# Performance work log

Measured on AMD Instinct MI355X. Metric: run time of the kernel, lower is better.

The kernel has to match this reference:

```python
import jax, jax.numpy as jnp
import numpy as np

B, S, D = 32, 512, 512
H, DK, DV, DFF = 8, 64, 64, 2048
TEMP = float(np.sqrt(DK))  # d_k ** 0.5
COS_EPS = 1e-8             # torch.cosine_similarity eps
LN_EPS = 1e-5


def _layernorm(x, g, b):
    mu = jnp.mean(x, axis=-1, keepdims=True)
    var = jnp.var(x, axis=-1, keepdims=True)
    return (x - mu) * jax.lax.rsqrt(var + LN_EPS) * g + b


def setup_inputs() -> dict:
    key = jax.random.key(0)
    ks = jax.random.split(key, 12)
    s = 0.02
    return {
        "x": jax.random.normal(ks[0], (B, S, D), dtype=jnp.float32),
        "w_q": jax.random.normal(ks[1], (D, H * DK), dtype=jnp.float32) * s,
        "w_k": jax.random.normal(ks[2], (D, H * DK), dtype=jnp.float32) * s,
        "w_v": jax.random.normal(ks[3], (D, H * DV), dtype=jnp.float32) * s,
        "w_o": jax.random.normal(ks[4], (H * DV, D), dtype=jnp.float32) * s,
        "w_ff1": jax.random.normal(ks[5], (D, DFF), dtype=jnp.float32) * s,
        "b_ff1": jnp.zeros((DFF,), dtype=jnp.float32),
        "w_ff2": jax.random.normal(ks[6], (DFF, D), dtype=jnp.float32) * s,
        "b_ff2": jnp.zeros((D,), dtype=jnp.float32),
        "g1": jnp.ones((D,), dtype=jnp.float32),
        "b1": jnp.zeros((D,), dtype=jnp.float32),
        "g2": jnp.ones((D,), dtype=jnp.float32),
        "b2": jnp.zeros((D,), dtype=jnp.float32),
    }


def reference(x, w_q, w_k, w_v, w_o, w_ff1, b_ff1, w_ff2, b_ff2, g1, b1, g2, b2):
    b, s, _ = x.shape
    # projections -> [b, h, s, d]
    q = (x @ w_q).reshape(b, s, H, DK).transpose(0, 2, 1, 3)
    k = (x @ w_k).reshape(b, s, H, DK).transpose(0, 2, 1, 3)
    v = (x @ w_v).reshape(b, s, H, DV).transpose(0, 2, 1, 3)
    # cosine-similarity attention: dot(q,k) / max(||q||*||k||, eps) / temperature
    scores = jnp.einsum("bhqd,bhkd->bhqk", q, k)
    nq = jnp.linalg.norm(q, axis=-1)  # [b,h,s]
    nk = jnp.linalg.norm(k, axis=-1)
    denom = jnp.maximum(nq[:, :, :, None] * nk[:, :, None, :], COS_EPS)
    attn = jax.nn.softmax(scores / denom / TEMP, axis=-1)
    out = jnp.einsum("bhqk,bhkd->bhqd", attn, v)  # [b,h,s,dv]
    out = out.transpose(0, 2, 1, 3).reshape(b, s, H * DV) @ w_o
    # residual + LN1
    h1 = _layernorm(x + out, g1, b1)
    # FFN
    ffn = jax.nn.relu(h1 @ w_ff1 + b_ff1) @ w_ff2 + b_ff2
    # residual + LN2
    return _layernorm(h1 + ffn, g2, b2)
```

## Files before the change

### kernel.cpp

```cpp
#include <hip/hip_runtime.h>
#include <cmath>

typedef __bf16 bf16x8 __attribute__((ext_vector_type(8)));
typedef float  floatx4 __attribute__((ext_vector_type(4)));

#define LN_EPS 1e-5f
#define COS_EPS 1e-8f
#define INV_TEMP 0.125f

static const int Mrows = 16384;

__device__ __forceinline__ void gload_lds16(const void* g, void* l) {
  __builtin_amdgcn_global_load_lds(
      (const __attribute__((address_space(1))) void*)g,
      (__attribute__((address_space(3))) void*)l, 16, 0, 0);
}

__global__ __launch_bounds__(256) void convert_bf16(const float* __restrict__ src,
                                                    __bf16* __restrict__ dst, int n4) {
  int i = blockIdx.x * 256 + threadIdx.x;
  if (i < n4) {
    float4 v = ((const float4*)src)[i];
    dst[i * 4 + 0] = (__bf16)v.x;
    dst[i * 4 + 1] = (__bf16)v.y;
    dst[i * 4 + 2] = (__bf16)v.z;
    dst[i * 4 + 3] = (__bf16)v.w;
  }
}

__global__ __launch_bounds__(256) void tr_kernel(const float* __restrict__ src,
                                                 __bf16* __restrict__ dst,
                                                 int R, int C) {
  __shared__ __bf16 til[64][72];
  const int tid = threadIdx.x;
  const int bx = blockIdx.x;
  const int by = blockIdx.y;
  const float* s = src + (size_t)(by * 64) * C + bx * 64;
  int r = tid >> 4, c4 = (tid & 15) * 4;
  for (int p = 0; p < 4; ++p) {
    int rr = r + p * 16;
    float4 v = *(const float4*)(s + (size_t)rr * C + c4);
    til[c4 + 0][rr] = (__bf16)v.x;
    til[c4 + 1][rr] = (__bf16)v.y;
    til[c4 + 2][rr] = (__bf16)v.z;
    til[c4 + 3][rr] = (__bf16)v.w;
  }
  __syncthreads();
  __bf16* d = dst + (size_t)(bx * 64) * R + by * 64;
  int orow = tid >> 3, oc8 = (tid & 7) * 8;
  for (int p = 0; p < 2; ++p) {
    int rr = orow + p * 32;
    *(bf16x8*)(d + (size_t)rr * R + oc8) = *(const bf16x8*)(&til[rr][oc8]);
  }
}

template <int EPI>
__global__ __launch_bounds__(256) void gemm_bt(const __bf16* __restrict__ A,
                                               const __bf16* __restrict__ Bt,
                                               void* __restrict__ Cv,
                                               void* __restrict__ Cv2,
                                               const float* __restrict__ bias,
                                               float* __restrict__ norms,
                                               int nbn, int Ndim, int Kdim, int kspan) {
  __shared__ __align__(16) __bf16 As[128 * 64];
  __shared__ __align__(16) __bf16 Bs[128 * 64];
  const int tid = threadIdx.x;
  const int wave = tid >> 6, lane = tid & 63;
  const int l15 = lane & 15, quad = lane >> 4;
  const int id = blockIdx.x;
  const int xcd = id & 7, t = id >> 3;
  const int nblk = t % nbn, mblk = (t / nbn) * 8 + xcd;
  const int m0 = mblk * 128, n0 = nblk * 128;
  const int k0 = blockIdx.z * kspan;
  const int wrow = (wave >> 1) * 64, wcol = (wave & 1) * 64;
  const int rs = lane >> 3;
  const int swz_st = ((lane & 7) ^ rs) * 8;
  const int s7 = l15 & 7;

  floatx4 zero = {0.f, 0.f, 0.f, 0.f};
  floatx4 acc[4][4];
  for (int i = 0; i < 4; ++i)
    for (int j = 0; j < 4; ++j) acc[i][j] = zero;

  for (int kt = k0; kt < k0 + kspan; kt += 64) {
    __syncthreads();
    for (int c = 0; c < 8; ++c) {
      int g = wave * 8 + c;
      const __bf16* src;
      __bf16* dst;
      if (g < 16) {
        int row = m0 + g * 8 + rs;
        src = A + (size_t)row * Kdim + kt + swz_st;
        dst = As + g * 512;
      } else {
        int g2 = g - 16;
        int row = n0 + g2 * 8 + rs;
        src = Bt + (size_t)row * Kdim + kt + swz_st;
        dst = Bs + g2 * 512;
      }
      gload_lds16(src, dst + lane * 8);
    }
    __syncthreads();
    for (int hh = 0; hh < 2; ++hh) {
      int ko = ((hh * 4 + quad) ^ s7) * 8;
      bf16x8 a[4], b[4];
      for (int i = 0; i < 4; ++i)
        a[i] = *(const bf16x8*)(As + (wrow + i * 16 + l15) * 64 + ko);
      for (int j = 0; j < 4; ++j)
        b[j] = *(const bf16x8*)(Bs + (wcol + j * 16 + l15) * 64 + ko);
      for (int i = 0; i < 4; ++i)
        for (int j = 0; j < 4; ++j)
          acc[i][j] = __builtin_amdgcn_mfma_f32_16x16x32_bf16(a[i], b[j], acc[i][j], 0, 0, 0);
    }
  }

  if (EPI == 4) {
    int head_global = (n0 + wcol) >> 6;
    int kind = head_global >> 3;
    if (kind < 2) {
      int h = head_global & 7;
      for (int i = 0; i < 4; ++i)
        for (int r = 0; r < 4; ++r) {
          float sq = 0.f;
          for (int j = 0; j < 4; ++j) {
            float v = acc[i][j][r];
            sq += v * v;
          }
          for (int m = 1; m < 16; m <<= 1) sq += __shfl_xor(sq, m, 64);
          if (l15 == 0) {
            int arow = m0 + wrow + i * 16 + quad * 4 + r;
            int bb = arow >> 9, ss = arow & 511;
            norms[kind * 131072 + ((bb << 3) + h) * 512 + ss] = sqrtf(sq);
          }
        }
    }
  }

  float* outp = (float*)Cv;
  if (EPI == 1 && blockIdx.z != 0) outp = (float*)Cv2;

  for (int i = 0; i < 4; ++i)
    for (int j = 0; j < 4; ++j) {
      int row = m0 + wrow + i * 16 + quad * 4;
      int col = n0 + wcol + j * 16 + l15;
      float bv = (EPI == 2) ? bias[col] : 0.f;
      for (int r = 0; r < 4; ++r) {
        float v = acc[i][j][r];
        size_t idx = (size_t)(row + r) * Ndim + col;
        if (EPI == 4) {
          ((__bf16*)Cv)[idx] = (__bf16)v;
        } else if (EPI == 1) {
          outp[idx] = v;
        } else {
          v += bv;
          v = v > 0.f ? v : 0.f;
          ((__bf16*)Cv)[idx] = (__bf16)v;
        }
      }
    }
}

__global__ __launch_bounds__(256) void vtrans_kernel(const __bf16* __restrict__ qkv,
                                                     __bf16* __restrict__ vtg) {
  __shared__ __align__(16) unsigned short til[64][68];
  const int tid = threadIdx.x;
  const int st = blockIdx.x;
  const int bh = blockIdx.y;
  const int b = bh >> 3, h = bh & 7;
  const unsigned short* src = (const unsigned short*)qkv +
      (size_t)(b * 512 + st * 64) * 1536 + 1024 + h * 64;
  for (int it = 0; it < 2; ++it) {
    int row = it * 32 + (tid >> 3);
    int c8 = (tid & 7) * 8;
    bf16x8 v = *(const bf16x8*)((const __bf16*)src + (size_t)row * 1536 + c8);
    for (int i = 0; i < 8; ++i) til[row][c8 + i] = ((unsigned short*)&v)[i];
  }
  __syncthreads();
  unsigned short* dst = (unsigned short*)vtg + (size_t)bh * 32768 + st * 64;
  for (int it = 0; it < 2; ++it) {
    int d = it * 32 + (tid >> 3);
    int s8 = (tid & 7) * 8;
    unsigned short v[8];
    for (int i = 0; i < 8; ++i) v[i] = til[s8 + i][d];
    *(bf16x8*)(dst + (size_t)d * 512 + s8) = *(bf16x8*)v;
  }
}

__global__ __launch_bounds__(256) void attn_kernel(const __bf16* __restrict__ qkv,
                                                   const __bf16* __restrict__ vtg,
                                                   const float* __restrict__ norms,
                                                   __bf16* __restrict__ out) {
  __shared__ __align__(16) __bf16 Ks[64 * 64];
  __shared__ __align__(16) __bf16 Vs[64 * 64];
  __shared__ __align__(16) __bf16 P[4][16 * 72];
  const int tid = threadIdx.x, wave = tid >> 6, lane = tid & 63;
  const int l15 = lane & 15, quad = lane >> 4;
  const int qh = blockIdx.x;
  const int bh = blockIdx.y;
  const int b = bh >> 3, h = bh & 7;
  const int qbase = qh * 256 + wave * 64;
  const int rs = lane >> 3;
  const int swz_st = ((lane & 7) ^ rs) * 8;
  const int s7 = l15 & 7;

  const __bf16* Qb = qkv + (size_t)(b * 512) * 1536 + h * 64;
  const __bf16* Kb = Qb + 512;
  const __bf16* Vtb = vtg + (size_t)bh * 32768;
  const float* nkbase = norms + 131072 + bh * 512;
  __bf16* Pw = P[wave];

  bf16x8 aq[4][2];
  float nq[4][4];
  for (int ch = 0; ch < 4; ++ch) {
    int qrow = qbase + ch * 16;
    aq[ch][0] = *(const bf16x8*)(Qb + (size_t)(qrow + l15) * 1536 + quad * 8);
    aq[ch][1] = *(const bf16x8*)(Qb + (size_t)(qrow + l15) * 1536 + 32 + quad * 8);
    for (int r = 0; r < 4; ++r) nq[ch][r] = norms[bh * 512 + qrow + quad * 4 + r];
  }

  floatx4 zero = {0.f, 0.f, 0.f, 0.f};
  floatx4 o[4][4];
  float lsum[4][4];
  for (int ch = 0; ch < 4; ++ch)
    for (int jd = 0; jd < 4; ++jd) o[ch][jd] = zero;
  for (int ch = 0; ch < 4; ++ch)
    for (int r = 0; r < 4; ++r) lsum[ch][r] = 0.f;

  for (int kt = 0; kt < 8; ++kt) {
    int s0 = kt * 64;
    __syncthreads();
    for (int c = 0; c < 4; ++c) {
      int g = wave * 4 + c;
      const __bf16* src;
      __bf16* dst;
      if (g < 8) {
        int sk = g * 8 + rs;
        src = Kb + (size_t)(s0 + sk) * 1536 + swz_st;
        dst = Ks + g * 512;
      } else {
        int g2 = g - 8;
        int d = g2 * 8 + rs;
        src = Vtb + (size_t)d * 512 + s0 + swz_st;
        dst = Vs + g2 * 512;
      }
      gload_lds16(src, dst + lane * 8);
    }
    __syncthreads();

    float nk[4];
    for (int j = 0; j < 4; ++j) nk[j] = nkbase[s0 + j * 16 + l15];

    for (int ch = 0; ch < 4; ++ch) {
      floatx4 z[4];
      for (int j = 0; j < 4; ++j) {
        int r64 = (j * 16 + l15) * 64;
        bf16x8 b0 = *(const bf16x8*)(Ks + r64 + ((quad ^ s7) * 8));
        bf16x8 b1 = *(const bf16x8*)(Ks + r64 + (((4 + quad) ^ s7) * 8));
        floatx4 zz = zero;
        zz = __builtin_amdgcn_mfma_f32_16x16x32_bf16(aq[ch][0], b0, zz, 0, 0, 0);
        zz = __builtin_amdgcn_mfma_f32_16x16x32_bf16(aq[ch][1], b1, zz, 0, 0, 0);
        z[j] = zz;
      }
      for (int j = 0; j < 4; ++j)
        for (int r = 0; r < 4; ++r) {
          float den = nq[ch][r] * nk[j];
          den = den > COS_EPS ? den : COS_EPS;
          float p = __expf(z[j][r] * __builtin_amdgcn_rcpf(den) * INV_TEMP);
          lsum[ch][r] += p;
          Pw[(quad * 4 + r) * 72 + j * 16 + l15] = (__bf16)p;
        }
      bf16x8 ap0 = *(const bf16x8*)(Pw + l15 * 72 + quad * 8);
      bf16x8 ap1 = *(const bf16x8*)(Pw + l15 * 72 + 32 + quad * 8);
      for (int jd = 0; jd < 4; ++jd) {
        int r64 = (jd * 16 + l15) * 64;
        bf16x8 v0 = *(const bf16x8*)(Vs + r64 + ((quad ^ s7) * 8));
        bf16x8 v1 = *(const bf16x8*)(Vs + r64 + (((4 + quad) ^ s7) * 8));
        o[ch][jd] = __builtin_amdgcn_mfma_f32_16x16x32_bf16(ap0, v0, o[ch][jd], 0, 0, 0);
        o[ch][jd] = __builtin_amdgcn_mfma_f32_16x16x32_bf16(ap1, v1, o[ch][jd], 0, 0, 0);
      }
    }
  }

  for (int ch = 0; ch < 4; ++ch)
    for (int r = 0; r < 4; ++r) {
      float s = lsum[ch][r];
      for (int m = 1; m < 16; m <<= 1) s += __shfl_xor(s, m, 64);
      lsum[ch][r] = __builtin_amdgcn_rcpf(s);
    }
  for (int ch = 0; ch < 4; ++ch)
    for (int jd = 0; jd < 4; ++jd)
      for (int r = 0; r < 4; ++r) {
        int q = qbase + ch * 16 + quad * 4 + r;
        int d = jd * 16 + l15;
        out[(size_t)(b * 512 + q) * 512 + h * 64 + d] = (__bf16)(o[ch][jd][r] * lsum[ch][r]);
      }
}

template <bool WB>
__global__ __launch_bounds__(256) void resid_ln(const float* __restrict__ X1,
                                                const float* __restrict__ X2,
                                                const float* __restrict__ X3,
                                                const float* __restrict__ bias,
                                                const float* __restrict__ g,
                                                const float* __restrict__ be,
                                                float* __restrict__ outf,
                                                __bf16* __restrict__ outb) {
  int row = blockIdx.x * 4 + (threadIdx.x >> 6);
  int lane = threadIdx.x & 63;
  const float4* r1 = (const float4*)(X1 + (size_t)row * 512);
  const float4* r2 = (const float4*)(X2 + (size_t)row * 512);
  float4 a = r1[lane], b = r2[lane];
  float4 cc = r1[lane + 64], d = r2[lane + 64];
  float v[8] = {a.x + b.x, a.y + b.y, a.z + b.z, a.w + b.w,
                cc.x + d.x, cc.y + d.y, cc.z + d.z, cc.w + d.w};
  if (X3) {
    const float4* r3 = (const float4*)(X3 + (size_t)row * 512);
    float4 e = r3[lane], f = r3[lane + 64];
    v[0] += e.x; v[1] += e.y; v[2] += e.z; v[3] += e.w;
    v[4] += f.x; v[5] += f.y; v[6] += f.z; v[7] += f.w;
  }
  if (bias) {
    float4 q0 = ((const float4*)bias)[lane], q1 = ((const float4*)bias)[lane + 64];
    v[0] += q0.x; v[1] += q0.y; v[2] += q0.z; v[3] += q0.w;
    v[4] += q1.x; v[5] += q1.y; v[6] += q1.z; v[7] += q1.w;
  }
  float s = 0.f, sq = 0.f;
  for (int i = 0; i < 8; ++i) {
    s += v[i];
    sq += v[i] * v[i];
  }
  for (int m = 1; m < 64; m <<= 1) {
    s += __shfl_xor(s, m, 64);
    sq += __shfl_xor(sq, m, 64);
  }
  float mean = s * (1.f / 512.f);
  float var = sq * (1.f / 512.f) - mean * mean;
  float rstd = rsqrtf(var + LN_EPS);
  float4 g0 = ((const float4*)g)[lane], g1 = ((const float4*)g)[lane + 64];
  float4 b0 = ((const float4*)be)[lane], b1 = ((const float4*)be)[lane + 64];
  float gg[8] = {g0.x, g0.y, g0.z, g0.w, g1.x, g1.y, g1.z, g1.w};
  float bb[8] = {b0.x, b0.y, b0.z, b0.w, b1.x, b1.y, b1.z, b1.w};
  float o[8];
  for (int i = 0; i < 8; ++i) o[i] = (v[i] - mean) * rstd * gg[i] + bb[i];
  float4 w0 = {o[0], o[1], o[2], o[3]}, w1 = {o[4], o[5], o[6], o[7]};
  ((float4*)(outf + (size_t)row * 512))[lane] = w0;
  ((float4*)(outf + (size_t)row * 512))[lane + 64] = w1;
  if (WB) {
    __bf16* ob = outb + (size_t)row * 512;
    for (int i = 0; i < 4; ++i) ob[lane * 4 + i] = (__bf16)o[i];
    for (int i = 0; i < 4; ++i) ob[256 + lane * 4 + i] = (__bf16)o[4 + i];
  }
}

extern "C" void kernel_launch(void* const* d_in, const int* in_sizes, int n_in,
                              void* d_out, int out_size, void* d_ws, size_t ws_size,
                              hipStream_t stream) {
  const float* x     = (const float*)d_in[0];
  const float* w_q   = (const float*)d_in[1];
  const float* w_k   = (const float*)d_in[2];
  const float* w_v   = (const float*)d_in[3];
  const float* w_o   = (const float*)d_in[4];
  const float* w_ff1 = (const float*)d_in[5];
  const float* b_ff1 = (const float*)d_in[6];
  const float* w_ff2 = (const float*)d_in[7];
  const float* b_ff2 = (const float*)d_in[8];
  const float* g1    = (const float*)d_in[9];
  const float* b1    = (const float*)d_in[10];
  const float* g2    = (const float*)d_in[11];
  const float* b2    = (const float*)d_in[12];
  float* out = (float*)d_out;

  char* ws = (char*)d_ws;
  size_t off = 0;
  auto alloc = [&](size_t bytes) -> void* {
    void* p = ws + off;
    off += (bytes + 255) & ~(size_t)255;
    return p;
  };
  __bf16* xb     = (__bf16*)alloc((size_t)Mrows * 512 * 2);
  __bf16* wt_qkv = (__bf16*)alloc((size_t)1536 * 512 * 2);
  __bf16* wt_o   = (__bf16*)alloc((size_t)512 * 512 * 2);
  __bf16* wt_ff1 = (__bf16*)alloc((size_t)2048 * 512 * 2);
  __bf16* wt_ff2 = (__bf16*)alloc((size_t)512 * 2048 * 2);
  __bf16* qkv    = (__bf16*)alloc((size_t)Mrows * 1536 * 2);
  float*  norms  = (float*)alloc((size_t)262144 * 4);
  __bf16* attn   = (__bf16*)alloc((size_t)Mrows * 512 * 2);
  float*  proj   = (float*)alloc((size_t)Mrows * 512 * 4);
  float*  h1f    = (float*)alloc((size_t)Mrows * 512 * 4);
  __bf16* h1b    = (__bf16*)alloc((size_t)Mrows * 512 * 2);
  __bf16* mid    = (__bf16*)alloc((size_t)Mrows * 2048 * 2);
  __bf16* vtg    = mid;
  float*  part1  = (float*)qkv;

  convert_bf16<<<8192, 256, 0, stream>>>(x, xb, Mrows * 512 / 4);
  tr_kernel<<<dim3(8, 8), 256, 0, stream>>>(w_q, wt_qkv, 512, 512);
  tr_kernel<<<dim3(8, 8), 256, 0, stream>>>(w_k, wt_qkv + 512 * 512, 512, 512);
  tr_kernel<<<dim3(8, 8), 256, 0, stream>>>(w_v, wt_qkv + 2 * 512 * 512, 512, 512);
  tr_kernel<<<dim3(8, 8), 256, 0, stream>>>(w_o, wt_o, 512, 512);
  tr_kernel<<<dim3(32, 8), 256, 0, stream>>>(w_ff1, wt_ff1, 512, 2048);
  tr_kernel<<<dim3(8, 32), 256, 0, stream>>>(w_ff2, wt_ff2, 2048, 512);

  gemm_bt<4><<<dim3(12 * 128), 256, 0, stream>>>(xb, wt_qkv, qkv, nullptr, nullptr,
                                                 norms, 12, 1536, 512, 512);
  vtrans_kernel<<<dim3(8, 256), 256, 0, stream>>>(qkv, vtg);
  attn_kernel<<<dim3(2, 256), 256, 0, stream>>>(qkv, vtg, norms, attn);
  gemm_bt<1><<<dim3(4 * 128), 256, 0, stream>>>(attn, wt_o, proj, nullptr, nullptr,
                                                nullptr, 4, 512, 512, 512);
  resid_ln<true><<<4096, 256, 0, stream>>>(x, proj, nullptr, nullptr, g1, b1, h1f, h1b);
  gemm_bt<2><<<dim3(16 * 128), 256, 0, stream>>>(h1b, wt_ff1, mid, nullptr, b_ff1,
                                                 nullptr, 16, 2048, 512, 512);
  gemm_bt<1><<<dim3(4 * 128, 1, 2), 256, 0, stream>>>(mid, wt_ff2, proj, part1, nullptr,
                                                      nullptr, 4, 512, 2048, 1024);
  resid_ln<false><<<4096, 256, 0, stream>>>(h1f, proj, part1, b_ff2, g2, b2, out, nullptr);
}
```

Before: 372.9 us.

## Merge prep kernels, drop FF2 split-K, and read h1 residual from bf16

Merges the x conversion and all six weight transposes into one prep kernel, which cuts the launch count. The FF2 GEMM loses its two-way split-K and runs over the full K of 2048 in one pass. The second LayerNorm now reads the h1 residual from the bf16 copy, so the fp32 h1 buffer is no longer stored or reloaded, and both LayerNorms use contiguous 8-element vector loads and stores. This saves memory traffic and launches, but the residual loses precision and the FF2 GEMM has half as many blocks, each doing a longer K loop.

```diff
diff --git a/kernel.cpp b/kernel.cpp
--- a/kernel.cpp
+++ b/kernel.cpp
@@ -16,25 +16,36 @@
       (__attribute__((address_space(3))) void*)l, 16, 0, 0);
 }
 
-__global__ __launch_bounds__(256) void convert_bf16(const float* __restrict__ src,
-                                                    __bf16* __restrict__ dst, int n4) {
-  int i = blockIdx.x * 256 + threadIdx.x;
-  if (i < n4) {
-    float4 v = ((const float4*)src)[i];
-    dst[i * 4 + 0] = (__bf16)v.x;
-    dst[i * 4 + 1] = (__bf16)v.y;
-    dst[i * 4 + 2] = (__bf16)v.z;
-    dst[i * 4 + 3] = (__bf16)v.w;
-  }
-}
-
-__global__ __launch_bounds__(256) void tr_kernel(const float* __restrict__ src,
-                                                 __bf16* __restrict__ dst,
-                                                 int R, int C) {
+__global__ __launch_bounds__(256) void prep_kernel(const float* __restrict__ x, __bf16* __restrict__ xb,
+                                                   const float* __restrict__ wq, const float* __restrict__ wk,
+                                                   const float* __restrict__ wv, const float* __restrict__ wo,
+                                                   const float* __restrict__ wff1, const float* __restrict__ wff2,
+                                                   __bf16* __restrict__ tq, __bf16* __restrict__ tk,
+                                                   __bf16* __restrict__ tv, __bf16* __restrict__ to_,
+                                                   __bf16* __restrict__ tff1, __bf16* __restrict__ tff2) {
+  const int bid = blockIdx.x, tid = threadIdx.x;
+  if (bid < 8192) {
+    int i = bid * 256 + tid;
+    float4 v = ((const float4*)x)[i];
+    __bf16* d = xb + i * 4;
+    d[0] = (__bf16)v.x; d[1] = (__bf16)v.y; d[2] = (__bf16)v.z; d[3] = (__bf16)v.w;
+    return;
+  }
   __shared__ __bf16 til[64][72];
-  const int tid = threadIdx.x;
-  const int bx = blockIdx.x;
-  const int by = blockIdx.y;
+  int t = bid - 8192;
+  const float* src; __bf16* dst; int R, C, bx, by;
+  if (t < 256) {
+    int w = t >> 6, tt = t & 63;
+    const float* srcs[4] = {wq, wk, wv, wo};
+    __bf16* dsts[4] = {tq, tk, tv, to_};
+    src = srcs[w]; dst = dsts[w]; R = 512; C = 512; bx = tt & 7; by = tt >> 3;
+  } else if (t < 512) {
+    int tt = t - 256;
+    src = wff1; dst = tff1; R = 512; C = 2048; bx = tt & 31; by = tt >> 5;
+  } else {
+    int tt = t - 512;
+    src = wff2; dst = tff2; R = 2048; C = 512; bx = tt & 7; by = tt >> 3;
+  }
   const float* s = src + (size_t)(by * 64) * C + bx * 64;
   int r = tid >> 4, c4 = (tid & 15) * 4;
   for (int p = 0; p < 4; ++p) {
@@ -58,10 +69,9 @@
 __global__ __launch_bounds__(256) void gemm_bt(const __bf16* __restrict__ A,
                                                const __bf16* __restrict__ Bt,
                                                void* __restrict__ Cv,
-                                               void* __restrict__ Cv2,
                                                const float* __restrict__ bias,
                                                float* __restrict__ norms,
-                                               int nbn, int Ndim, int Kdim, int kspan) {
+                                               int nbn, int Ndim, int Kdim) {
   __shared__ __align__(16) __bf16 As[128 * 64];
   __shared__ __align__(16) __bf16 Bs[128 * 64];
   const int tid = threadIdx.x;
@@ -71,7 +81,6 @@
   const int xcd = id & 7, t = id >> 3;
   const int nblk = t % nbn, mblk = (t / nbn) * 8 + xcd;
   const int m0 = mblk * 128, n0 = nblk * 128;
-  const int k0 = blockIdx.z * kspan;
   const int wrow = (wave >> 1) * 64, wcol = (wave & 1) * 64;
   const int rs = lane >> 3;
   const int swz_st = ((lane & 7) ^ rs) * 8;
@@ -82,7 +91,7 @@
   for (int i = 0; i < 4; ++i)
     for (int j = 0; j < 4; ++j) acc[i][j] = zero;
 
-  for (int kt = k0; kt < k0 + kspan; kt += 64) {
+  for (int kt = 0; kt < Kdim; kt += 64) {
     __syncthreads();
     for (int c = 0; c < 8; ++c) {
       int g = wave * 8 + c;
@@ -136,9 +145,6 @@
     }
   }
 
-  float* outp = (float*)Cv;
-  if (EPI == 1 && blockIdx.z != 0) outp = (float*)Cv2;
-
   for (int i = 0; i < 4; ++i)
     for (int j = 0; j < 4; ++j) {
       int row = m0 + wrow + i * 16 + quad * 4;
@@ -150,7 +156,7 @@
         if (EPI == 4) {
           ((__bf16*)Cv)[idx] = (__bf16)v;
         } else if (EPI == 1) {
-          outp[idx] = v;
+          ((float*)Cv)[idx] = v;
         } else {
           v += bv;
           v = v > 0.f ? v : 0.f;
@@ -296,10 +302,10 @@
       }
 }
 
-template <bool WB>
-__global__ __launch_bounds__(256) void resid_ln(const float* __restrict__ X1,
+template <bool X1BF, bool WF, bool WB>
+__global__ __launch_bounds__(256) void resid_ln(const float* __restrict__ X1f,
+                                                const __bf16* __restrict__ X1b,
                                                 const float* __restrict__ X2,
-                                                const float* __restrict__ X3,
                                                 const float* __restrict__ bias,
                                                 const float* __restrict__ g,
                                                 const float* __restrict__ be,
@@ -307,22 +313,25 @@
                                                 __bf16* __restrict__ outb) {
   int row = blockIdx.x * 4 + (threadIdx.x >> 6);
   int lane = threadIdx.x & 63;
-  const float4* r1 = (const float4*)(X1 + (size_t)row * 512);
-  const float4* r2 = (const float4*)(X2 + (size_t)row * 512);
-  float4 a = r1[lane], b = r2[lane];
-  float4 cc = r1[lane + 64], d = r2[lane + 64];
-  float v[8] = {a.x + b.x, a.y + b.y, a.z + b.z, a.w + b.w,
-                cc.x + d.x, cc.y + d.y, cc.z + d.z, cc.w + d.w};
-  if (X3) {
-    const float4* r3 = (const float4*)(X3 + (size_t)row * 512);
-    float4 e = r3[lane], f = r3[lane + 64];
-    v[0] += e.x; v[1] += e.y; v[2] += e.z; v[3] += e.w;
-    v[4] += f.x; v[5] += f.y; v[6] += f.z; v[7] += f.w;
-  }
-  if (bias) {
-    float4 q0 = ((const float4*)bias)[lane], q1 = ((const float4*)bias)[lane + 64];
-    v[0] += q0.x; v[1] += q0.y; v[2] += q0.z; v[3] += q0.w;
-    v[4] += q1.x; v[5] += q1.y; v[6] += q1.z; v[7] += q1.w;
+  float v[8];
+  if (X1BF) {
+    bf16x8 a = *(const bf16x8*)(X1b + (size_t)row * 512 + lane * 8);
+    for (int i = 0; i < 8; ++i) v[i] = (float)a[i];
+    const float4* r2 = (const float4*)(X2 + (size_t)row * 512);
+    float4 b0 = r2[lane * 2], b1 = r2[lane * 2 + 1];
+    v[0] += b0.x; v[1] += b0.y; v[2] += b0.z; v[3] += b0.w;
+    v[4] += b1.x; v[5] += b1.y; v[6] += b1.z; v[7] += b1.w;
+    if (bias) {
+      const float* bp = bias + lane * 8;
+      for (int i = 0; i < 8; ++i) v[i] += bp[i];
+    }
+  } else {
+    const float4* r1 = (const float4*)(X1f + (size_t)row * 512);
+    const float4* r2 = (const float4*)(X2 + (size_t)row * 512);
+    float4 a0 = r1[lane * 2], a1 = r1[lane * 2 + 1];
+    float4 b0 = r2[lane * 2], b1 = r2[lane * 2 + 1];
+    v[0] = a0.x + b0.x; v[1] = a0.y + b0.y; v[2] = a0.z + b0.z; v[3] = a0.w + b0.w;
+    v[4] = a1.x + b1.x; v[5] = a1.y + b1.y; v[6] = a1.z + b1.z; v[7] = a1.w + b1.w;
   }
   float s = 0.f, sq = 0.f;
   for (int i = 0; i < 8; ++i) {
@@ -336,19 +345,19 @@
   float mean = s * (1.f / 512.f);
   float var = sq * (1.f / 512.f) - mean * mean;
   float rstd = rsqrtf(var + LN_EPS);
-  float4 g0 = ((const float4*)g)[lane], g1 = ((const float4*)g)[lane + 64];
-  float4 b0 = ((const float4*)be)[lane], b1 = ((const float4*)be)[lane + 64];
-  float gg[8] = {g0.x, g0.y, g0.z, g0.w, g1.x, g1.y, g1.z, g1.w};
-  float bb[8] = {b0.x, b0.y, b0.z, b0.w, b1.x, b1.y, b1.z, b1.w};
+  const float* gp = g + lane * 8;
+  const float* bp2 = be + lane * 8;
   float o[8];
-  for (int i = 0; i < 8; ++i) o[i] = (v[i] - mean) * rstd * gg[i] + bb[i];
-  float4 w0 = {o[0], o[1], o[2], o[3]}, w1 = {o[4], o[5], o[6], o[7]};
-  ((float4*)(outf + (size_t)row * 512))[lane] = w0;
-  ((float4*)(outf + (size_t)row * 512))[lane + 64] = w1;
+  for (int i = 0; i < 8; ++i) o[i] = (v[i] - mean) * rstd * gp[i] + bp2[i];
+  if (WF) {
+    float4 w0 = {o[0], o[1], o[2], o[3]}, w1 = {o[4], o[5], o[6], o[7]};
+    ((float4*)(outf + (size_t)row * 512))[lane * 2] = w0;
+    ((float4*)(outf + (size_t)row * 512))[lane * 2 + 1] = w1;
+  }
   if (WB) {
-    __bf16* ob = outb + (size_t)row * 512;
-    for (int i = 0; i < 4; ++i) ob[lane * 4 + i] = (__bf16)o[i];
-    for (int i = 0; i < 4; ++i) ob[256 + lane * 4 + i] = (__bf16)o[4 + i];
+    __bf16 tmp[8];
+    for (int i = 0; i < 8; ++i) tmp[i] = (__bf16)o[i];
+    *(bf16x8*)(outb + (size_t)row * 512 + lane * 8) = *(bf16x8*)tmp;
   }
 }
 
@@ -386,30 +395,26 @@
   float*  norms  = (float*)alloc((size_t)262144 * 4);
   __bf16* attn   = (__bf16*)alloc((size_t)Mrows * 512 * 2);
   float*  proj   = (float*)alloc((size_t)Mrows * 512 * 4);
-  float*  h1f    = (float*)alloc((size_t)Mrows * 512 * 4);
   __bf16* h1b    = (__bf16*)alloc((size_t)Mrows * 512 * 2);
   __bf16* mid    = (__bf16*)alloc((size_t)Mrows * 2048 * 2);
   __bf16* vtg    = mid;
-  float*  part1  = (float*)qkv;
-
-  convert_bf16<<<8192, 256, 0, stream>>>(x, xb, Mrows * 512 / 4);
-  tr_kernel<<<dim3(8, 8), 256, 0, stream>>>(w_q, wt_qkv, 512, 512);
-  tr_kernel<<<dim3(8, 8), 256, 0, stream>>>(w_k, wt_qkv + 512 * 512, 512, 512);
-  tr_kernel<<<dim3(8, 8), 256, 0, stream>>>(w_v, wt_qkv + 2 * 512 * 512, 512, 512);
-  tr_kernel<<<dim3(8, 8), 256, 0, stream>>>(w_o, wt_o, 512, 512);
-  tr_kernel<<<dim3(32, 8), 256, 0, stream>>>(w_ff1, wt_ff1, 512, 2048);
-  tr_kernel<<<dim3(8, 32), 256, 0, stream>>>(w_ff2, wt_ff2, 2048, 512);
-
-  gemm_bt<4><<<dim3(12 * 128), 256, 0, stream>>>(xb, wt_qkv, qkv, nullptr, nullptr,
-                                                 norms, 12, 1536, 512, 512);
+
+  prep_kernel<<<8960, 256, 0, stream>>>(x, xb, w_q, w_k, w_v, w_o, w_ff1, w_ff2,
+                                        wt_qkv, wt_qkv + 512 * 512, wt_qkv + 2 * 512 * 512,
+                                        wt_o, wt_ff1, wt_ff2);
+
+  gemm_bt<4><<<dim3(12 * 128), 256, 0, stream>>>(xb, wt_qkv, qkv, nullptr,
+                                                 norms, 12, 1536, 512);
   vtrans_kernel<<<dim3(8, 256), 256, 0, stream>>>(qkv, vtg);
   attn_kernel<<<dim3(2, 256), 256, 0, stream>>>(qkv, vtg, norms, attn);
-  gemm_bt<1><<<dim3(4 * 128), 256, 0, stream>>>(attn, wt_o, proj, nullptr, nullptr,
-                                                nullptr, 4, 512, 512, 512);
-  resid_ln<true><<<4096, 256, 0, stream>>>(x, proj, nullptr, nullptr, g1, b1, h1f, h1b);
-  gemm_bt<2><<<dim3(16 * 128), 256, 0, stream>>>(h1b, wt_ff1, mid, nullptr, b_ff1,
-                                                 nullptr, 16, 2048, 512, 512);
-  gemm_bt<1><<<dim3(4 * 128, 1, 2), 256, 0, stream>>>(mid, wt_ff2, proj, part1, nullptr,
-                                                      nullptr, 4, 512, 2048, 1024);
-  resid_ln<false><<<4096, 256, 0, stream>>>(h1f, proj, part1, b_ff2, g2, b2, out, nullptr);
-}
+  gemm_bt<1><<<dim3(4 * 128), 256, 0, stream>>>(attn, wt_o, proj, nullptr,
+                                                nullptr, 4, 512, 512);
+  resid_ln<false, false, true><<<4096, 256, 0, stream>>>(x, nullptr, proj, nullptr,
+                                                         g1, b1, nullptr, h1b);
+  gemm_bt<2><<<dim3(16 * 128), 256, 0, stream>>>(h1b, wt_ff1, mid, b_ff1,
+                                                 nullptr, 16, 2048, 512);
+  gemm_bt<1><<<dim3(4 * 128), 256, 0, stream>>>(mid, wt_ff2, proj, nullptr,
+                                                nullptr, 4, 512, 2048);
+  resid_ln<true, true, false><<<4096, 256, 0, stream>>>(nullptr, h1b, proj, b_ff2,
+                                                        g2, b2, out, nullptr);
+}
```

After: 349.2 us. -6.4%, faster.
